# Optimization experiments

Measured on AMD Instinct MI355X. Metric: run time of the kernel, lower is better.

Reference implementation:

```python
import jax, jax.numpy as jnp
import numpy as np

B, C = 4096, 1024  # batch_size, label_size (== embedding_dim of dense outputs)


def setup_inputs() -> dict:
    key = jax.random.key(0)
    k1, k2, k3 = jax.random.split(key, 3)
    return {
        "outs": jax.random.normal(k1, (B, C), dtype=jnp.float32),
        "class_centers": jax.random.normal(k2, (C, C), dtype=jnp.float32),
        "batch_label": jax.random.randint(k3, (B,), 0, C, dtype=jnp.int32),
    }


def reference(outs, class_centers, batch_label):
    b, c = outs.shape
    # ---- standard cross-entropy (F.cross_entropy, mean reduction) ----
    logp = jax.nn.log_softmax(outs, axis=-1)
    ce = -jnp.mean(jnp.take_along_axis(logp, batch_label[:, None].astype(jnp.int32), axis=1))

    # ---- InfoNCE with Wasserstein hard-negative mining ----
    # memory bank stores detached embeddings -> centers carry no gradient
    centers = jax.lax.stop_gradient(class_centers)
    pos = centers[batch_label]  # [B, C] positive per anchor

    # calculate_2_wasserstein_dist on 1-D vectors reduces EXACTLY to
    # ||x - y||^2 - 2*d*sqrt(1e-15)  (covariance terms vanish for a single column)
    const = jnp.float32(-2.0 * c * np.sqrt(1e-15))
    x = jax.lax.stop_gradient(outs)  # similarity used only for index selection
    sq = jnp.sum(x * x, axis=-1)  # [B]
    sim = sq[:, None] + sq[None, :] - 2.0 * (x @ x.T) + const  # [B, B]

    # negatives: different label (self automatically excluded: same label)
    mask = batch_label[:, None] != batch_label[None, :]  # [B, B]
    neg_inf = jnp.float32(-1e30)
    # hard negative: largest wasserstein distance among negatives (topk k=1)
    hard_idx = jnp.argmax(jnp.where(mask, sim, neg_inf), axis=1)  # [B]
    # random negative: uniform over negatives via Gumbel-max (torch randperm analogue)
    g = jax.random.gumbel(jax.random.key(42), (b, b), dtype=jnp.float32)
    rand_idx = jnp.argmax(jnp.where(mask, g, neg_inf), axis=1)  # [B]

    pos_sim = jnp.sum(outs * pos, axis=-1)                # [B]
    n_rand = jnp.sum(outs * outs[rand_idx], axis=-1)      # [B]
    n_hard = jnp.sum(outs * outs[hard_idx], axis=-1)      # [B]
    logits = jnp.stack([pos_sim, n_rand, n_hard], axis=1)  # [B, 1+num_negatives]
    info_nce = -jnp.mean(jax.nn.log_softmax(logits, axis=1)[:, 0])

    return ce + 0.1 * info_nce
```

## Files before the change

### kernel.cpp

```cpp
#include <hip/hip_runtime.h>
#include <hip/hip_bf16.h>
#include <stdint.h>

#define Bsz 4096
#define Csz 1024

typedef __attribute__((ext_vector_type(8))) short short8;
typedef __attribute__((ext_vector_type(4))) float f32x4;

__device__ __forceinline__ unsigned fenc(float v) {
  unsigned u = __float_as_uint(v);
  return (u & 0x80000000u) ? ~u : (u | 0x80000000u);
}

__device__ __forceinline__ void load_lds16(const void* g, void* l) {
  __builtin_amdgcn_global_load_lds(
      (const __attribute__((address_space(1))) void*)g,
      (__attribute__((address_space(3))) void*)l, 16, 0, 0);
}

__device__ __forceinline__ uint32_t rotl32(uint32_t x, int r) {
  return (x << r) | (x >> (32 - r));
}

__global__ __launch_bounds__(256) void k_rowstats(
    const float* __restrict__ outs, const int* __restrict__ label,
    unsigned short* __restrict__ xb, float* __restrict__ sq,
    float* __restrict__ ce) {
  const int row = blockIdx.x;
  const int tid = threadIdx.x;
  const int lane = tid & 63, wid = tid >> 6;
  const float4 v = reinterpret_cast<const float4*>(outs + (size_t)row * Csz)[tid];

  ushort4 u4;
  {
    __hip_bfloat16 h;
    h = __float2bfloat16(v.x); u4.x = *reinterpret_cast<const unsigned short*>(&h);
    h = __float2bfloat16(v.y); u4.y = *reinterpret_cast<const unsigned short*>(&h);
    h = __float2bfloat16(v.z); u4.z = *reinterpret_cast<const unsigned short*>(&h);
    h = __float2bfloat16(v.w); u4.w = *reinterpret_cast<const unsigned short*>(&h);
  }
  reinterpret_cast<ushort4*>(xb + (size_t)row * Csz)[tid] = u4;

  __shared__ float wred[3][4];
  float mx = fmaxf(fmaxf(v.x, v.y), fmaxf(v.z, v.w));
#pragma unroll
  for (int off = 32; off; off >>= 1) mx = fmaxf(mx, __shfl_xor(mx, off, 64));
  if (lane == 0) wred[0][wid] = mx;
  __syncthreads();
  mx = fmaxf(fmaxf(wred[0][0], wred[0][1]), fmaxf(wred[0][2], wred[0][3]));

  float se = expf(v.x - mx) + expf(v.y - mx) + expf(v.z - mx) + expf(v.w - mx);
  float s2 = v.x * v.x + v.y * v.y + v.z * v.z + v.w * v.w;
#pragma unroll
  for (int off = 32; off; off >>= 1) {
    se += __shfl_xor(se, off, 64);
    s2 += __shfl_xor(s2, off, 64);
  }
  if (lane == 0) { wred[1][wid] = se; wred[2][wid] = s2; }
  __syncthreads();
  if (tid == 0) {
    const float set = wred[1][0] + wred[1][1] + wred[1][2] + wred[1][3];
    const float sqt = wred[2][0] + wred[2][1] + wred[2][2] + wred[2][3];
    sq[row] = sqt;
    ce[row] = -(outs[(size_t)row * Csz + label[row]] - mx - logf(set));
  }
}

__global__ __launch_bounds__(256) void k_hard(
    const unsigned short* __restrict__ xb, const float* __restrict__ sq,
    const int* __restrict__ label, unsigned long long* __restrict__ hard) {
  __shared__ unsigned short As[128 * 64];
  __shared__ unsigned short Bs[128 * 64];
  const int bi = blockIdx.x >> 5, bj = blockIdx.x & 31;
  const int tid = threadIdx.x;
  const int wid = tid >> 6, lane = tid & 63;
  const int wr = wid >> 1, wc = wid & 1;

  f32x4 acc[4][4];
#pragma unroll
  for (int m = 0; m < 4; ++m)
#pragma unroll
    for (int n = 0; n < 4; ++n) acc[m][n] = (f32x4){0.f, 0.f, 0.f, 0.f};

  const unsigned short* Ag = xb + (size_t)(bi * 128) * Csz;
  const unsigned short* Bg = xb + (size_t)(bj * 128) * Csz;
  const int lrow = lane >> 3;
  const int lch = (lane & 7) * 8;

  for (int kt = 0; kt < Csz; kt += 64) {
#pragma unroll
    for (int c = 0; c < 4; ++c) {
      const int r = wid * 32 + c * 8;
      load_lds16(Ag + (size_t)(r + lrow) * Csz + kt + lch, &As[r * 64]);
      load_lds16(Bg + (size_t)(r + lrow) * Csz + kt + lch, &Bs[r * 64]);
    }
    __syncthreads();
#pragma unroll
    for (int ks = 0; ks < 2; ++ks) {
      const int kb = ks * 32 + (lane >> 4) * 8;
      short8 a[4], b[4];
#pragma unroll
      for (int m = 0; m < 4; ++m)
        a[m] = *reinterpret_cast<const short8*>(
            &As[(wr * 64 + m * 16 + (lane & 15)) * 64 + kb]);
#pragma unroll
      for (int n = 0; n < 4; ++n)
        b[n] = *reinterpret_cast<const short8*>(
            &Bs[(wc * 64 + n * 16 + (lane & 15)) * 64 + kb]);
#pragma unroll
      for (int m = 0; m < 4; ++m)
#pragma unroll
        for (int n = 0; n < 4; ++n)
          acc[m][n] = __builtin_amdgcn_mfma_f32_16x16x32_bf16(a[m], b[n], acc[m][n], 0, 0, 0);
    }
    __syncthreads();
  }

  const float cst = -2.0f * 1024.0f * 3.1622776601683794e-8f;
#pragma unroll
  for (int m = 0; m < 4; ++m) {
#pragma unroll
    for (int r = 0; r < 4; ++r) {
      const int i = bi * 128 + wr * 64 + m * 16 + (lane >> 4) * 4 + r;
      const int li = label[i];
      const float sqi = sq[i];
      float bestv = -3.0e38f;
      int bestj = 0x7FFFFFFF;
#pragma unroll
      for (int n = 0; n < 4; ++n) {
        const int j = bj * 128 + wc * 64 + n * 16 + (lane & 15);
        const float val = sqi + sq[j] - 2.0f * acc[m][n][r] + cst;
        if (label[j] != li && val > bestv) { bestv = val; bestj = j; }
      }
      unsigned long long pack =
          (bestj == 0x7FFFFFFF)
              ? 0ull
              : (((unsigned long long)fenc(bestv)) << 32) | (unsigned)(~bestj);
#pragma unroll
      for (int off = 1; off < 16; off <<= 1) {
        unsigned long long o = __shfl_xor(pack, off, 64);
        if (o > pack) pack = o;
      }
      if ((lane & 15) == 0 && pack) atomicMax(&hard[i], pack);
    }
  }
}

__global__ __launch_bounds__(256) void k_rand(
    const int* __restrict__ label, int* __restrict__ ridx) {
  const int i = blockIdx.x;
  const int tid = threadIdx.x;
  const int lane = tid & 63, wid = tid >> 6;
  const int li0 = label[i], li1 = label[i + 2048];
  const uint32_t k1c = 42u, k2c = 0x1BD11BDAu ^ 42u;
  unsigned long long b0 = 0ull, b1 = 0ull;
  for (int j = tid; j < Bsz; j += 256) {
    uint32_t x0 = (uint32_t)(i * Bsz + j);
    uint32_t x1 = x0 + 8388608u;
    x1 += k1c;
#define RND(rt) { x0 += x1; x1 = rotl32(x1, rt); x1 ^= x0; }
    RND(13) RND(15) RND(26) RND(6)
    x0 += k1c; x1 += k2c + 1u;
    RND(17) RND(29) RND(16) RND(24)
    x0 += k2c; x1 += 2u;
    RND(13) RND(15) RND(26) RND(6)
    x1 += k1c + 3u;
    RND(17) RND(29) RND(16) RND(24)
    x0 += k1c; x1 += k2c + 4u;
    RND(13) RND(15) RND(26) RND(6)
    x0 += k2c; x1 += 5u;
#undef RND
    const int lj = label[j];
    if (lj != li0) {
      unsigned long long p = (((unsigned long long)(x0 >> 9)) << 32) | (uint32_t)(~j);
      if (p > b0) b0 = p;
    }
    if (lj != li1) {
      unsigned long long p = (((unsigned long long)(x1 >> 9)) << 32) | (uint32_t)(~j);
      if (p > b1) b1 = p;
    }
  }
#pragma unroll
  for (int off = 32; off; off >>= 1) {
    unsigned long long o0 = __shfl_xor(b0, off, 64); if (o0 > b0) b0 = o0;
    unsigned long long o1 = __shfl_xor(b1, off, 64); if (o1 > b1) b1 = o1;
  }
  __shared__ unsigned long long r0[4], r1[4];
  if (lane == 0) { r0[wid] = b0; r1[wid] = b1; }
  __syncthreads();
  if (tid == 0) {
#pragma unroll
    for (int w = 1; w < 4; ++w) {
      if (r0[w] > b0) b0 = r0[w];
      if (r1[w] > b1) b1 = r1[w];
    }
    ridx[i] = (int)(~(uint32_t)b0);
    ridx[i + 2048] = (int)(~(uint32_t)b1);
  }
}

__global__ __launch_bounds__(256) void k_nce(
    const float* __restrict__ outs, const float* __restrict__ centers,
    const int* __restrict__ label, const unsigned long long* __restrict__ hard,
    const int* __restrict__ ridx, float* __restrict__ nce) {
  const int i = blockIdx.x;
  const int tid = threadIdx.x;
  const int lane = tid & 63, wid = tid >> 6;
  const int li = label[i];
  const int jh = (int)(~(uint32_t)hard[i]);
  const int jr = ridx[i];
  const float4 a  = reinterpret_cast<const float4*>(outs + (size_t)i * Csz)[tid];
  const float4 c  = reinterpret_cast<const float4*>(centers + (size_t)li * Csz)[tid];
  const float4 rr = reinterpret_cast<const float4*>(outs + (size_t)jr * Csz)[tid];
  const float4 hh = reinterpret_cast<const float4*>(outs + (size_t)jh * Csz)[tid];
  float dp = a.x * c.x + a.y * c.y + a.z * c.z + a.w * c.w;
  float dr = a.x * rr.x + a.y * rr.y + a.z * rr.z + a.w * rr.w;
  float dh = a.x * hh.x + a.y * hh.y + a.z * hh.z + a.w * hh.w;
#pragma unroll
  for (int off = 32; off; off >>= 1) {
    dp += __shfl_xor(dp, off, 64);
    dr += __shfl_xor(dr, off, 64);
    dh += __shfl_xor(dh, off, 64);
  }
  __shared__ float w0[4], w1[4], w2[4];
  if (lane == 0) { w0[wid] = dp; w1[wid] = dr; w2[wid] = dh; }
  __syncthreads();
  if (tid == 0) {
    const float l0 = w0[0] + w0[1] + w0[2] + w0[3];
    const float l1 = w1[0] + w1[1] + w1[2] + w1[3];
    const float l2 = w2[0] + w2[1] + w2[2] + w2[3];
    const float m = fmaxf(l0, fmaxf(l1, l2));
    const float lse = logf(expf(l0 - m) + expf(l1 - m) + expf(l2 - m));
    nce[i] = -(l0 - m - lse);
  }
}

__global__ __launch_bounds__(1024) void k_final(
    const float* __restrict__ ce, const float* __restrict__ nce,
    float* __restrict__ out) {
  __shared__ double s[1024];
  const int tid = threadIdx.x;
  double v = 0.0;
#pragma unroll
  for (int q = 0; q < 4; ++q) {
    v += (double)ce[tid + q * 1024];
    v += 0.1 * (double)nce[tid + q * 1024];
  }
  s[tid] = v;
  __syncthreads();
  for (int off = 512; off; off >>= 1) {
    if (tid < off) s[tid] += s[tid + off];
    __syncthreads();
  }
  if (tid == 0) out[0] = (float)(s[0] / 4096.0);
}

extern "C" void kernel_launch(void* const* d_in, const int* in_sizes, int n_in,
                              void* d_out, int out_size, void* d_ws, size_t ws_size,
                              hipStream_t stream) {
  const float* outs = (const float*)d_in[0];
  const float* centers = (const float*)d_in[1];
  const int* label = (const int*)d_in[2];
  float* out = (float*)d_out;

  char* ws = (char*)d_ws;
  unsigned short* xb = (unsigned short*)ws;
  unsigned long long* hard = (unsigned long long*)(ws + (8u << 20));
  float* sq = (float*)(ws + (8u << 20) + 32768);
  float* ce = sq + Bsz;
  float* nce = ce + Bsz;
  int* ridx = (int*)(nce + Bsz);

  hipMemsetAsync(hard, 0, Bsz * sizeof(unsigned long long), stream);
  k_rowstats<<<Bsz, 256, 0, stream>>>(outs, label, xb, sq, ce);
  k_hard<<<1024, 256, 0, stream>>>(xb, sq, label, hard);
  k_rand<<<Bsz / 2, 256, 0, stream>>>(label, ridx);
  k_nce<<<Bsz, 256, 0, stream>>>(outs, centers, label, hard, ridx, nce);
  k_final<<<1, 1024, 0, stream>>>(ce, nce, out);
}
```

Baseline: 179.2 us.

## Fuse rand and memset into rowstats; retile hard GEMM to 256x256 double-buffered

Merges the Gumbel random-negative kernel and the memset of the hard buffer into the row-stats kernel, which removes two launches. The hard-negative Gram kernel moves from 128x128 tiles with 256 threads to 256x256 tiles with 512 threads. It also adds double-buffered LDS staging with an XOR swizzle to avoid bank conflicts, a grouped block-index swizzle for L2 reuse, and setprio around the MFMAs. The larger tiles mean only 256 blocks, which may leave some CUs idle, and use more registers and LDS per block.

```diff
diff --git a/kernel.cpp b/kernel.cpp
--- a/kernel.cpp
+++ b/kernel.cpp
@@ -26,7 +26,8 @@
 __global__ __launch_bounds__(256) void k_rowstats(
     const float* __restrict__ outs, const int* __restrict__ label,
     unsigned short* __restrict__ xb, float* __restrict__ sq,
-    float* __restrict__ ce) {
+    float* __restrict__ ce, unsigned long long* __restrict__ hard,
+    int* __restrict__ ridx) {
   const int row = blockIdx.x;
   const int tid = threadIdx.x;
   const int lane = tid & 63, wid = tid >> 6;
@@ -64,94 +65,12 @@
     const float sqt = wred[2][0] + wred[2][1] + wred[2][2] + wred[2][3];
     sq[row] = sqt;
     ce[row] = -(outs[(size_t)row * Csz + label[row]] - mx - logf(set));
-  }
-}
-
-__global__ __launch_bounds__(256) void k_hard(
-    const unsigned short* __restrict__ xb, const float* __restrict__ sq,
-    const int* __restrict__ label, unsigned long long* __restrict__ hard) {
-  __shared__ unsigned short As[128 * 64];
-  __shared__ unsigned short Bs[128 * 64];
-  const int bi = blockIdx.x >> 5, bj = blockIdx.x & 31;
-  const int tid = threadIdx.x;
-  const int wid = tid >> 6, lane = tid & 63;
-  const int wr = wid >> 1, wc = wid & 1;
-
-  f32x4 acc[4][4];
-#pragma unroll
-  for (int m = 0; m < 4; ++m)
-#pragma unroll
-    for (int n = 0; n < 4; ++n) acc[m][n] = (f32x4){0.f, 0.f, 0.f, 0.f};
-
-  const unsigned short* Ag = xb + (size_t)(bi * 128) * Csz;
-  const unsigned short* Bg = xb + (size_t)(bj * 128) * Csz;
-  const int lrow = lane >> 3;
-  const int lch = (lane & 7) * 8;
-
-  for (int kt = 0; kt < Csz; kt += 64) {
-#pragma unroll
-    for (int c = 0; c < 4; ++c) {
-      const int r = wid * 32 + c * 8;
-      load_lds16(Ag + (size_t)(r + lrow) * Csz + kt + lch, &As[r * 64]);
-      load_lds16(Bg + (size_t)(r + lrow) * Csz + kt + lch, &Bs[r * 64]);
-    }
-    __syncthreads();
-#pragma unroll
-    for (int ks = 0; ks < 2; ++ks) {
-      const int kb = ks * 32 + (lane >> 4) * 8;
-      short8 a[4], b[4];
-#pragma unroll
-      for (int m = 0; m < 4; ++m)
-        a[m] = *reinterpret_cast<const short8*>(
-            &As[(wr * 64 + m * 16 + (lane & 15)) * 64 + kb]);
-#pragma unroll
-      for (int n = 0; n < 4; ++n)
-        b[n] = *reinterpret_cast<const short8*>(
-            &Bs[(wc * 64 + n * 16 + (lane & 15)) * 64 + kb]);
-#pragma unroll
-      for (int m = 0; m < 4; ++m)
-#pragma unroll
-        for (int n = 0; n < 4; ++n)
-          acc[m][n] = __builtin_amdgcn_mfma_f32_16x16x32_bf16(a[m], b[n], acc[m][n], 0, 0, 0);
-    }
-    __syncthreads();
-  }
-
-  const float cst = -2.0f * 1024.0f * 3.1622776601683794e-8f;
-#pragma unroll
-  for (int m = 0; m < 4; ++m) {
-#pragma unroll
-    for (int r = 0; r < 4; ++r) {
-      const int i = bi * 128 + wr * 64 + m * 16 + (lane >> 4) * 4 + r;
-      const int li = label[i];
-      const float sqi = sq[i];
-      float bestv = -3.0e38f;
-      int bestj = 0x7FFFFFFF;
-#pragma unroll
-      for (int n = 0; n < 4; ++n) {
-        const int j = bj * 128 + wc * 64 + n * 16 + (lane & 15);
-        const float val = sqi + sq[j] - 2.0f * acc[m][n][r] + cst;
-        if (label[j] != li && val > bestv) { bestv = val; bestj = j; }
-      }
-      unsigned long long pack =
-          (bestj == 0x7FFFFFFF)
-              ? 0ull
-              : (((unsigned long long)fenc(bestv)) << 32) | (unsigned)(~bestj);
-#pragma unroll
-      for (int off = 1; off < 16; off <<= 1) {
-        unsigned long long o = __shfl_xor(pack, off, 64);
-        if (o > pack) pack = o;
-      }
-      if ((lane & 15) == 0 && pack) atomicMax(&hard[i], pack);
-    }
-  }
-}
-
-__global__ __launch_bounds__(256) void k_rand(
-    const int* __restrict__ label, int* __restrict__ ridx) {
-  const int i = blockIdx.x;
-  const int tid = threadIdx.x;
-  const int lane = tid & 63, wid = tid >> 6;
+    hard[row] = 0ull;
+  }
+
+  if (row >= 2048) return;
+
+  const int i = row;
   const int li0 = label[i], li1 = label[i + 2048];
   const uint32_t k1c = 42u, k2c = 0x1BD11BDAu ^ 42u;
   unsigned long long b0 = 0ull, b1 = 0ull;
@@ -200,6 +119,116 @@
   }
 }
 
+__global__ __launch_bounds__(512, 2) void k_hard(
+    const unsigned short* __restrict__ xb, const float* __restrict__ sq,
+    const int* __restrict__ label, unsigned long long* __restrict__ hard) {
+  __shared__ unsigned short As[2][256 * 64];
+  __shared__ unsigned short Bs[2][256 * 64];
+
+  const int bid = (int)blockIdx.x;
+  const int swz = (bid & 7) * 32 + (bid >> 3);
+  const int bi = swz >> 4, bj = swz & 15;
+
+  const int tid = (int)threadIdx.x;
+  const int wid = tid >> 6, lane = tid & 63;
+  const int wm = wid >> 2;
+  const int wn = wid & 3;
+  const int fr = lane & 15;
+  const int fq = lane >> 4;
+  const int sx = lane & 7;
+
+  f32x4 acc[8][4];
+#pragma unroll
+  for (int m = 0; m < 8; ++m)
+#pragma unroll
+    for (int n = 0; n < 4; ++n) acc[m][n] = (f32x4){0.f, 0.f, 0.f, 0.f};
+
+  const unsigned short* Ag = xb + (size_t)(bi * 256) * Csz;
+  const unsigned short* Bg = xb + (size_t)(bj * 256) * Csz;
+  const int lrow = lane >> 3;
+  const int lch = ((lane & 7) ^ lrow) * 8;
+
+  auto STAGE = [&](int buf, int kt) {
+#pragma unroll
+    for (int c = 0; c < 4; ++c) {
+      const int r = wid * 32 + c * 8;
+      load_lds16(Ag + (size_t)(r + lrow) * Csz + kt + lch, &As[buf][r * 64]);
+      load_lds16(Bg + (size_t)(r + lrow) * Csz + kt + lch, &Bs[buf][r * 64]);
+    }
+  };
+  auto COMPUTE = [&](int buf) {
+#pragma unroll
+    for (int kh = 0; kh < 2; ++kh) {
+      const int choff = ((kh * 4 + fq) ^ sx) * 8;
+      short8 a[8], b[4];
+#pragma unroll
+      for (int m = 0; m < 8; ++m)
+        a[m] = *reinterpret_cast<const short8*>(
+            &As[buf][(wm * 128 + m * 16 + fr) * 64 + choff]);
+#pragma unroll
+      for (int n = 0; n < 4; ++n)
+        b[n] = *reinterpret_cast<const short8*>(
+            &Bs[buf][(wn * 64 + n * 16 + fr) * 64 + choff]);
+      __builtin_amdgcn_s_setprio(1);
+#pragma unroll
+      for (int m = 0; m < 8; ++m)
+#pragma unroll
+        for (int n = 0; n < 4; ++n)
+          acc[m][n] = __builtin_amdgcn_mfma_f32_16x16x32_bf16(a[m], b[n], acc[m][n], 0, 0, 0);
+      __builtin_amdgcn_s_setprio(0);
+    }
+  };
+
+  STAGE(0, 0);
+  STAGE(1, 64);
+#pragma unroll 1
+  for (int t = 0; t < 14; ++t) {
+    asm volatile("s_waitcnt vmcnt(8)" ::: "memory");
+    __builtin_amdgcn_s_barrier();
+    COMPUTE(t & 1);
+    asm volatile("s_waitcnt lgkmcnt(0)" ::: "memory");
+    __builtin_amdgcn_sched_barrier(0);
+    __builtin_amdgcn_s_barrier();
+    STAGE(t & 1, (t + 2) * 64);
+  }
+  asm volatile("s_waitcnt vmcnt(8)" ::: "memory");
+  __builtin_amdgcn_s_barrier();
+  COMPUTE(0);
+  asm volatile("s_waitcnt vmcnt(0)" ::: "memory");
+  __builtin_amdgcn_s_barrier();
+  COMPUTE(1);
+
+  const float cst = -2.0f * 1024.0f * 3.1622776601683794e-8f;
+
+#pragma unroll
+  for (int m = 0; m < 8; ++m) {
+#pragma unroll
+    for (int r = 0; r < 4; ++r) {
+      const int i = bi * 256 + wm * 128 + m * 16 + fq * 4 + r;
+      const int li = label[i];
+      const float sqi = sq[i];
+      float bestv = -3.0e38f;
+      int bestj = 0x7FFFFFFF;
+#pragma unroll
+      for (int n = 0; n < 4; ++n) {
+        const int j = bj * 256 + wn * 64 + n * 16 + fr;
+        const float val = sqi + sq[j] - 2.0f * acc[m][n][r] + cst;
+        if (label[j] != li && val > bestv) { bestv = val; bestj = j; }
+      }
+      unsigned long long pack =
+          (bestj == 0x7FFFFFFF)
+              ? 0ull
+              : (((unsigned long long)fenc(bestv)) << 32) | (unsigned)(~bestj);
+#pragma unroll
+      for (int off = 1; off < 16; off <<= 1) {
+        unsigned long long o = __shfl_xor(pack, off, 64);
+        if (o > pack) pack = o;
+      }
+      if (fr == 0 && pack) atomicMax(&hard[i], pack);
+    }
+  }
+}
+
 __global__ __launch_bounds__(256) void k_nce(
     const float* __restrict__ outs, const float* __restrict__ centers,
     const int* __restrict__ label, const unsigned long long* __restrict__ hard,
@@ -272,10 +301,8 @@
   float* nce = ce + Bsz;
   int* ridx = (int*)(nce + Bsz);
 
-  hipMemsetAsync(hard, 0, Bsz * sizeof(unsigned long long), stream);
-  k_rowstats<<<Bsz, 256, 0, stream>>>(outs, label, xb, sq, ce);
-  k_hard<<<1024, 256, 0, stream>>>(xb, sq, label, hard);
-  k_rand<<<Bsz / 2, 256, 0, stream>>>(label, ridx);
+  k_rowstats<<<Bsz, 256, 0, stream>>>(outs, label, xb, sq, ce, hard, ridx);
+  k_hard<<<256, 512, 0, stream>>>(xb, sq, label, hard);
   k_nce<<<Bsz, 256, 0, stream>>>(outs, centers, label, hard, ridx, nce);
   k_final<<<1, 1024, 0, stream>>>(ce, nce, out);
 }
```

New measurement: 157.7 us. -12.0%, faster.
